# Optimization experiments

Hardware: AMD Instinct MI355X
Metric: run time of the kernel (lower is better)

The kernel has to match this reference:

```python
import jax, jax.numpy as jnp
import numpy as np

B, T, D, H, OUT, VOCAB = 64, 100, 1024, 1024, 28, 28


def setup_inputs() -> dict:
    key = jax.random.key(0)
    ks = jax.random.split(key, 12)
    s = 0.05
    return {
        "x": jax.random.normal(ks[0], (B, T, D), jnp.float32),
        # encoder GRU (keras reset_after=True): kernel [D,3H], recurrent [H,3H], bias [2,3H]
        "enc_W": jax.random.normal(ks[1], (D, 3 * H), jnp.float32) * s,
        "enc_U": jax.random.normal(ks[2], (H, 3 * H), jnp.float32) * s,
        "enc_b": jax.random.normal(ks[3], (2, 3 * H), jnp.float32) * s,
        # AdditiveAttention learned scale vector [H]
        "att_scale": jax.random.normal(ks[4], (H,), jnp.float32) * s,
        # Embedding(28, H)
        "emb_W": jax.random.normal(ks[5], (VOCAB, H), jnp.float32) * s,
        # decoder GRUCell
        "dec_W": jax.random.normal(ks[6], (H, 3 * H), jnp.float32) * s,
        "dec_U": jax.random.normal(ks[7], (H, 3 * H), jnp.float32) * s,
        "dec_b": jax.random.normal(ks[8], (2, 3 * H), jnp.float32) * s,
        # fc: Dense(OUT) on concat([h, context]) -> [2H, OUT]
        "fc_W": jax.random.normal(ks[9], (2 * H, OUT), jnp.float32) * s,
        "fc_b": jax.random.normal(ks[10], (OUT,), jnp.float32) * s,
    }


def _gru_update(x_t, h, W, U, b):
    # keras GRU math with reset_after=True
    mx = x_t @ W + b[0]          # [B,3H]
    mi = h @ U + b[1]            # [B,3H]
    xz, xr, xh = jnp.split(mx, 3, axis=-1)
    rz, rr, rh = jnp.split(mi, 3, axis=-1)
    z = jax.nn.sigmoid(xz + rz)
    r = jax.nn.sigmoid(xr + rr)
    hh = jnp.tanh(xh + r * rh)
    return z * h + (1.0 - z) * hh


def reference(x, enc_W, enc_U, enc_b, att_scale, emb_W, dec_W, dec_U, dec_b, fc_W, fc_b):
    b, t, _ = x.shape
    h = jnp.zeros((b, enc_U.shape[0]), x.dtype)

    # encoder GRU, return_sequences=True
    def enc_step(h, x_t):
        h = _gru_update(x_t, h, enc_W, enc_U, enc_b)
        return h, h

    _, hpe = jax.lax.scan(enc_step, h, jnp.swapaxes(x, 0, 1))  # [T,B,H]
    hpe = jnp.swapaxes(hpe, 0, 1)                              # [B,T,H]

    out_dim = fc_b.shape[0]
    p0 = jnp.zeros((b, out_dim), x.dtype)
    h0 = jnp.zeros((b, dec_U.shape[0]), x.dtype)

    def dec_step(carry, _):
        p, hd = carry
        # additive attention: scores[b,j] = sum_d scale[d]*tanh(q[b,d]+k[b,j,d])
        scores = jnp.einsum('bth,h->bt', jnp.tanh(hd[:, None, :] + hpe), att_scale)
        attn = jax.nn.softmax(scores, axis=-1)
        ctx = jnp.einsum('bt,bth->bh', attn, hpe)
        idx = jnp.argmax(p, axis=-1)          # [B] int
        e = emb_W[idx]                        # [B,H]
        hd = _gru_update(e, hd, dec_W, dec_U, dec_b)
        p = jnp.concatenate([hd, ctx], axis=1) @ fc_W + fc_b
        return (p, hd), p

    _, outs = jax.lax.scan(dec_step, (p0, h0), None, length=t)  # [T,B,OUT]
    return jnp.swapaxes(outs, 0, 1)                              # [B,T,OUT]
```

## Files before the change

### kernel.cpp

```cpp
#include <hip/hip_runtime.h>

#define TT 100
#define HH 1024
#define H3 3072
#define NOUT 28

#define AGENT __HIP_MEMORY_SCOPE_AGENT
#define WGRP  __HIP_MEMORY_SCOPE_WORKGROUP
#define SPIN_CAP (1u<<20)

__device__ __forceinline__ float frcp_(float x){ return __builtin_amdgcn_rcpf(x); }
__device__ __forceinline__ float fsig_(float x){ return frcp_(1.0f + __expf(-x)); }
__device__ __forceinline__ float ftanh_(float x){ return 1.0f - 2.0f*frcp_(__expf(2.0f*x) + 1.0f); }

__device__ __forceinline__ unsigned long long aload8(const unsigned long long* p){
    return __hip_atomic_load(p, __ATOMIC_RELAXED, AGENT);
}
__device__ __forceinline__ unsigned aload4(const int* p){
    return (unsigned)__hip_atomic_load(p, __ATOMIC_RELAXED, AGENT);
}

__device__ __forceinline__ void gridbar(int* slot, int sub, int target){
    __syncthreads();
    if (threadIdx.x == 0){
        __hip_atomic_fetch_add(slot + sub*16, 1, __ATOMIC_RELAXED, AGENT);
        unsigned gy = 0; int s;
        do {
            s = 0;
            #pragma unroll
            for (int c=0;c<16;c++) s += __hip_atomic_load(slot + c*16, __ATOMIC_RELAXED, AGENT);
            if (s < target){ if (++gy > SPIN_CAP) break; __builtin_amdgcn_s_sleep(1); }
        } while (s < target);
    }
    __syncthreads();
}

__device__ __forceinline__ void wbar4(int* c, int tgt){
    asm volatile("s_waitcnt lgkmcnt(0)" ::: "memory");
    if ((threadIdx.x & 63) == 0) __hip_atomic_fetch_add(c, 1, __ATOMIC_RELAXED, WGRP);
    unsigned gy = 0;
    while (__hip_atomic_load(c, __ATOMIC_RELAXED, WGRP) < tgt){ if (++gy > SPIN_CAP) break; }
    asm volatile("" ::: "memory");
}

__global__ void k_init(int* ib, int n){
    int g = blockIdx.x*256 + threadIdx.x;
    if (g < n) ib[g] = 0;
}

__global__ __launch_bounds__(256) void k_transpose(const float* __restrict__ U0,
                                                   const float* __restrict__ U1,
                                                   float* __restrict__ T0,
                                                   float* __restrict__ T1){
    const float* U = blockIdx.z ? U1 : U0;
    float*       T = blockIdx.z ? T1 : T0;
    __shared__ float tile[32][33];
    int tx = threadIdx.x & 31, ty = threadIdx.x >> 5;
    int j0 = blockIdx.x*32, k0 = blockIdx.y*32;
    #pragma unroll
    for (int q=0;q<4;q++){
        int kr = ty + q*8;
        tile[kr][tx] = U[(size_t)(k0+kr)*H3 + j0 + tx];
    }
    __syncthreads();
    #pragma unroll
    for (int q=0;q<4;q++){
        int jr = ty + q*8;
        T[(size_t)(j0+jr)*HH + k0 + tx] = tile[tx][jr];
    }
}

__global__ __launch_bounds__(256) void k_edec(const float* __restrict__ emb,
                                              const float* __restrict__ W,
                                              const float* __restrict__ b0,
                                              float* __restrict__ E){
    int gid = blockIdx.x*256 + threadIdx.x;
    int v = gid / H3, j = gid - v*H3;
    float acc = b0[j];
    const float* er = emb + (size_t)v*HH;
    #pragma unroll 4
    for (int k=0;k<HH;k++) acc = fmaf(er[k], W[(size_t)k*H3 + j], acc);
    E[gid] = acc;
}

__global__ __launch_bounds__(256) void k_mxgemm(const float* __restrict__ A,
                                                const float* __restrict__ W,
                                                const float* __restrict__ b0,
                                                float* __restrict__ MXT){
    __shared__ float aT[32*68];
    __shared__ float bL[32*68];
    int tid = threadIdx.x;
    int row0 = blockIdx.y*64, col0 = blockIdx.x*64;
    int arow = tid>>2, acs = (tid&3)*4;
    int bk   = tid>>3, bcs = (tid&7)*4;
    int ty = tid>>4, tx = tid&15;
    float acc[4][4] = {};
    for (int kk=0; kk<HH; kk+=32){
        #pragma unroll
        for (int i=0;i<2;i++){
            int c = acs + i*16;
            float4 v = *(const float4*)(A + (size_t)(row0+arow)*HH + kk + c);
            aT[(c+0)*68 + arow] = v.x; aT[(c+1)*68 + arow] = v.y;
            aT[(c+2)*68 + arow] = v.z; aT[(c+3)*68 + arow] = v.w;
        }
        #pragma unroll
        for (int i=0;i<2;i++){
            int c = bcs + i*32;
            float4 v = *(const float4*)(W + (size_t)(kk+bk)*H3 + col0 + c);
            *(float4*)(bL + bk*68 + c) = v;
        }
        __syncthreads();
        #pragma unroll
        for (int k=0;k<32;k++){
            float4 a4 = *(const float4*)(aT + k*68 + ty*4);
            float4 b4 = *(const float4*)(bL + k*68 + tx*4);
            acc[0][0]=fmaf(a4.x,b4.x,acc[0][0]); acc[0][1]=fmaf(a4.x,b4.y,acc[0][1]);
            acc[0][2]=fmaf(a4.x,b4.z,acc[0][2]); acc[0][3]=fmaf(a4.x,b4.w,acc[0][3]);
            acc[1][0]=fmaf(a4.y,b4.x,acc[1][0]); acc[1][1]=fmaf(a4.y,b4.y,acc[1][1]);
            acc[1][2]=fmaf(a4.y,b4.z,acc[1][2]); acc[1][3]=fmaf(a4.y,b4.w,acc[1][3]);
            acc[2][0]=fmaf(a4.z,b4.x,acc[2][0]); acc[2][1]=fmaf(a4.z,b4.y,acc[2][1]);
            acc[2][2]=fmaf(a4.z,b4.z,acc[2][2]); acc[2][3]=fmaf(a4.z,b4.w,acc[2][3]);
            acc[3][0]=fmaf(a4.w,b4.x,acc[3][0]); acc[3][1]=fmaf(a4.w,b4.y,acc[3][1]);
            acc[3][2]=fmaf(a4.w,b4.z,acc[3][2]); acc[3][3]=fmaf(a4.w,b4.w,acc[3][3]);
        }
        __syncthreads();
    }
    float4 bb = *(const float4*)(b0 + col0 + tx*4);
    #pragma unroll
    for (int i=0;i<4;i++){
        int r = row0 + ty*4 + i;
        int bq = r / 100; int tq = r - bq*100;
        float v0 = acc[i][0] + bb.x, v1 = acc[i][1] + bb.y;
        float v2 = acc[i][2] + bb.z, v3 = acc[i][3] + bb.w;
        float* dst = MXT + ((size_t)tq*H3 + col0 + tx*4)*64 + bq;
        dst[0]   = v0; dst[64]  = v1; dst[128] = v2; dst[192] = v3;
    }
}

__global__ __launch_bounds__(256) void k_enc(const float* __restrict__ MXT,
                                             const float* __restrict__ Ut,
                                             const float* __restrict__ b1,
                                             float* __restrict__ hpe,
                                             float* __restrict__ hT,
                                             int* __restrict__ bar){
    __shared__ float hs[2][16384];
    int tid = threadIdx.x, lane = tid & 63;
    int wg = blockIdx.x;
    int sub = wg & 15;
    int cu = __builtin_amdgcn_readfirstlane(wg*4 + (tid>>6));
    const float* Uz = Ut + (size_t)cu*HH;
    const float* Ur = Uz + (size_t)HH*HH;
    const float* Uh = Ur + (size_t)HH*HH;
    float bz = b1[cu], br = b1[cu+HH], bh = b1[cu+2*HH];
    for (int t=0; t<TT; ++t){
        int cur = t & 1;
        const float* mx = MXT + (size_t)t*H3*64;
        float xz = mx[(size_t)cu*64 + lane];
        float xr = mx[(size_t)(cu+HH)*64 + lane];
        float xh = mx[(size_t)(cu+2*HH)*64 + lane];
        float az=0.f, ar=0.f, ah=0.f, hp=0.f;
        if (t > 0){
            const unsigned long long* g8 = (const unsigned long long*)(hT + (size_t)cur*65536);
            unsigned long long sv[32];
            #pragma unroll
            for (int s=0;s<32;s++) sv[s] = aload8(g8 + s*256 + tid);
            #pragma unroll
            for (int s=0;s<32;s++) ((unsigned long long*)hs[0])[s*256 + tid] = sv[s];
            __syncthreads();
            for (int q=0;q<4;++q){
                if (q<3){
                    #pragma unroll
                    for (int s=0;s<32;s++) sv[s] = aload8(g8 + (q+1)*8192 + s*256 + tid);
                }
                const float* hb = hs[q&1];
                const float* Uzq = Uz + q*256;
                const float* Urq = Ur + q*256;
                const float* Uhq = Uh + q*256;
                #pragma unroll 8
                for (int k=0;k<256;++k){
                    float h = hb[k*64 + lane];
                    az = fmaf(h, Uzq[k], az);
                    ar = fmaf(h, Urq[k], ar);
                    ah = fmaf(h, Uhq[k], ah);
                }
                if ((cu>>8) == q) hp = hb[(cu&255)*64 + lane];
                if (q<3){
                    #pragma unroll
                    for (int s=0;s<32;s++) ((unsigned long long*)hs[(q+1)&1])[s*256 + tid] = sv[s];
                }
                __syncthreads();
            }
        }
        float z  = fsig_(xz + az + bz);
        float r  = fsig_(xr + ar + br);
        float hh = ftanh_(xh + r*(ah + bh));
        float hnew = z*hp + (1.f - z)*hh;
        __hip_atomic_store(hT + (size_t)(cur^1)*65536 + cu*64 + lane, hnew, __ATOMIC_RELAXED, AGENT);
        hpe[((size_t)lane*TT + t)*HH + cu] = hnew;
        gridbar(bar + (size_t)t*256, sub, 256);
    }
}

__global__ __launch_bounds__(512) void k_dec(const float* __restrict__ hpe,
                                             const float* __restrict__ Ut,
                                             const float* __restrict__ b1,
                                             const float* __restrict__ Edec,
                                             const float* __restrict__ scale,
                                             const float* __restrict__ fcW,
                                             const float* __restrict__ fcb,
                                             float* __restrict__ hdT,
                                             float* __restrict__ hdl,
                                             float* __restrict__ out,
                                             int* __restrict__ idx_t,
                                             int* __restrict__ bar,
                                             int* __restrict__ flagidx){
    __shared__ float hs[2][16384];
    __shared__ float ctxs[4][1024];
    __shared__ float m_s[4], S_s[4];
    __shared__ int c_a, c_fc, go, cstg;
    int tid = threadIdx.x, wg = blockIdx.x;
    if (tid == 0){ c_a=0; c_fc=0; go=0; cstg=0; }
    __syncthreads();

    if (tid < 256){
        int lane = tid & 63;
        int sub = wg & 15;
        int cu = __builtin_amdgcn_readfirstlane(wg*4 + (tid>>6));
        const float* Uz = Ut + (size_t)cu*HH;
        const float* Ur = Uz + (size_t)HH*HH;
        const float* Uh = Ur + (size_t)HH*HH;
        float bz = b1[cu], br = b1[cu+HH], bh = b1[cu+2*HH];
        int stgt = 0;
        for (int i=0; i<TT; ++i){
            int cur = i & 1;
            float az=0.f, ar=0.f, ah=0.f, hp=0.f;
            if (i > 0){
                const unsigned long long* g8 = (const unsigned long long*)(hdT + (size_t)cur*65536);
                unsigned long long sv[32];
                #pragma unroll
                for (int s=0;s<32;s++) sv[s] = aload8(g8 + s*256 + tid);
                #pragma unroll
                for (int s=0;s<32;s++) ((unsigned long long*)hs[0])[s*256 + tid] = sv[s];
                wbar4(&cstg, stgt += 4);
                for (int q=0;q<4;++q){
                    if (q<3){
                        #pragma unroll
                        for (int s=0;s<32;s++) sv[s] = aload8(g8 + (q+1)*8192 + s*256 + tid);
                    }
                    const float* hb = hs[q&1];
                    const float* Uzq = Uz + q*256;
                    const float* Urq = Ur + q*256;
                    const float* Uhq = Uh + q*256;
                    #pragma unroll 8
                    for (int k=0;k<256;++k){
                        float h = hb[k*64 + lane];
                        az = fmaf(h, Uzq[k], az);
                        ar = fmaf(h, Urq[k], ar);
                        ah = fmaf(h, Uhq[k], ah);
                    }
                    if ((cu>>8) == q) hp = hb[(cu&255)*64 + lane];
                    if (q<3){
                        #pragma unroll
                        for (int s=0;s<32;s++) ((unsigned long long*)hs[(q+1)&1])[s*256 + tid] = sv[s];
                    }
                    wbar4(&cstg, stgt += 4);
                }
            }
            if (tid == 0){
                unsigned gy = 0; int s;
                do {
                    s = 0;
                    #pragma unroll
                    for (int c=0;c<8;c++) s += __hip_atomic_load(flagidx + (size_t)i*128 + c*16, __ATOMIC_RELAXED, AGENT);
                    if (s < 64){ if (++gy > SPIN_CAP) break; __builtin_amdgcn_s_sleep(1); }
                } while (s < 64);
                __hip_atomic_store(&go, i+1, __ATOMIC_RELAXED, WGRP);
            }
            { unsigned gy=0; while (__hip_atomic_load(&go, __ATOMIC_RELAXED, WGRP) < i+1){ if (++gy > SPIN_CAP) break; } }
            asm volatile("" ::: "memory");
            unsigned mi = aload4(idx_t + (size_t)i*64 + lane);
            if (mi > 27u) mi = 0;
            const float* ed = Edec + (size_t)mi*H3;
            float xz = ed[cu], xr = ed[cu+HH], xh = ed[cu+2*HH];
            float z  = fsig_(xz + az + bz);
            float r  = fsig_(xr + ar + br);
            float hh = ftanh_(xh + r*(ah + bh));
            float hnew = z*hp + (1.f - z)*hh;
            __hip_atomic_store(hdT + (size_t)(cur^1)*65536 + cu*64 + lane, hnew, __ATOMIC_RELAXED, AGENT);
            __hip_atomic_store(hdl + (size_t)(cur^1)*65536 + (size_t)lane*HH + cu, hnew, __ATOMIC_RELAXED, AGENT);
            gridbar(bar + (size_t)i*256, sub, 256);
        }
    } else if (wg < 64){
        int t2 = tid - 256;
        int w = t2 >> 6, lane = t2 & 63, b = wg;
        float sc[16];
        #pragma unroll
        for (int s4=0;s4<4;s4++){
            float4 v = *(const float4*)(scale + lane*16 + s4*4);
            sc[s4*4+0]=v.x; sc[s4*4+1]=v.y; sc[s4*4+2]=v.z; sc[s4*4+3]=v.w;
        }
        int j0 = w*25;
        for (int i=0; i<TT; ++i){
            float q[16];
            if (i == 0){
                #pragma unroll
                for (int d=0;d<16;d++) q[d]=0.f;
            } else {
                const unsigned long long* hq8 = (const unsigned long long*)(hdl + (size_t)(i&1)*65536 + (size_t)b*HH) + lane*8;
                #pragma unroll
                for (int s8=0;s8<8;s8++){
                    unsigned long long v = aload8(hq8 + s8);
                    q[2*s8+0] = __uint_as_float((unsigned)v);
                    q[2*s8+1] = __uint_as_float((unsigned)(v>>32));
                }
            }
            if (w == 0){
                if (i > 0){
                    float acc[NOUT];
                    #pragma unroll
                    for (int o=0;o<NOUT;o++) acc[o]=0.f;
                    float cv[16];
                    #pragma unroll
                    for (int s4=0;s4<4;s4++){
                        float4 c0 = ((const float4*)ctxs[0])[lane*4+s4];
                        float4 c1 = ((const float4*)ctxs[1])[lane*4+s4];
                        float4 c2 = ((const float4*)ctxs[2])[lane*4+s4];
                        float4 c3 = ((const float4*)ctxs[3])[lane*4+s4];
                        cv[s4*4+0]=c0.x+c1.x+c2.x+c3.x;
                        cv[s4*4+1]=c0.y+c1.y+c2.y+c3.y;
                        cv[s4*4+2]=c0.z+c1.z+c2.z+c3.z;
                        cv[s4*4+3]=c0.w+c1.w+c2.w+c3.w;
                    }
                    #pragma unroll
                    for (int dd=0;dd<16;++dd){
                        int d = lane*16 + dd;
                        const float* w0p = fcW + (size_t)d*NOUT;
                        const float* w1p = fcW + (size_t)(d+HH)*NOUT;
                        float hv=q[dd], cvv=cv[dd];
                        #pragma unroll
                        for (int o=0;o<NOUT;o++) acc[o] = fmaf(hv, w0p[o], fmaf(cvv, w1p[o], acc[o]));
                    }
                    #pragma unroll
                    for (int o=0;o<NOUT;o++){
                        #pragma unroll
                        for (int m=1;m<64;m<<=1) acc[o] += __shfl_xor(acc[o], m);
                    }
                    float bv=-3.0e38f; int bi=0;
                    #pragma unroll
                    for (int o=0;o<NOUT;o++){
                        float p = acc[o] + fcb[o];
                        acc[o] = p;
                        if (p > bv){ bv = p; bi = o; }
                    }
                    float vout = 0.f;
                    #pragma unroll
                    for (int o=0;o<NOUT;o++) if (lane == o) vout = acc[o];
                    if (lane < NOUT) out[((size_t)b*TT + (i-1))*NOUT + lane] = vout;
                    if (lane == 0){
                        __hip_atomic_store(idx_t + (size_t)i*64 + b, bi, __ATOMIC_RELAXED, AGENT);
                        asm volatile("s_waitcnt vmcnt(0)" ::: "memory");
                    }
                }
                if (lane == 0){
                    __hip_atomic_fetch_add(flagidx + (size_t)i*128 + (b&7)*16, 1, __ATOMIC_RELAXED, AGENT);
                    __hip_atomic_fetch_add(&c_fc, 1, __ATOMIC_RELAXED, WGRP);
                }
            }
            float m = -3.0e38f, S = 0.f;
            float a[16];
            #pragma unroll
            for (int d=0;d<16;d++) a[d]=0.f;
            for (int jj=0;jj<25;jj++){
                int j = j0 + jj;
                const float* hpj = hpe + ((size_t)b*TT + j)*HH + lane*16;
                float va[16];
                {
                    float4 v0 = *(const float4*)(hpj);
                    float4 v1 = *(const float4*)(hpj+4);
                    float4 v2 = *(const float4*)(hpj+8);
                    float4 v3 = *(const float4*)(hpj+12);
                    va[0]=v0.x;va[1]=v0.y;va[2]=v0.z;va[3]=v0.w;
                    va[4]=v1.x;va[5]=v1.y;va[6]=v1.z;va[7]=v1.w;
                    va[8]=v2.x;va[9]=v2.y;va[10]=v2.z;va[11]=v2.w;
                    va[12]=v3.x;va[13]=v3.y;va[14]=v3.z;va[15]=v3.w;
                }
                float s = 0.f;
                #pragma unroll
                for (int d=0;d<16;d++) s += sc[d]*ftanh_(q[d] + va[d]);
                #pragma unroll
                for (int mm=1;mm<64;mm<<=1) s += __shfl_xor(s, mm);
                float mn = fmaxf(m, s);
                float fold = __expf(m - mn);
                float e = __expf(s - mn);
                S = S*fold + e;
                #pragma unroll
                for (int d=0;d<16;d++) a[d] = a[d]*fold + e*va[d];
                m = mn;
            }
            if (lane == 0){ m_s[w] = m; S_s[w] = S; }
            asm volatile("s_waitcnt lgkmcnt(0)" ::: "memory");
            if (lane == 0) __hip_atomic_fetch_add(&c_a, 1, __ATOMIC_RELAXED, WGRP);
            { unsigned gy=0; while (__hip_atomic_load(&c_a, __ATOMIC_RELAXED, WGRP) < 4*(i+1)){ if (++gy > SPIN_CAP) break; } }
            asm volatile("" ::: "memory");
            float M = fmaxf(fmaxf(m_s[0],m_s[1]), fmaxf(m_s[2],m_s[3]));
            float St = S_s[0]*__expf(m_s[0]-M) + S_s[1]*__expf(m_s[1]-M)
                     + S_s[2]*__expf(m_s[2]-M) + S_s[3]*__expf(m_s[3]-M);
            float g = __expf(m - M) * frcp_(St);
            { unsigned gy=0; while (__hip_atomic_load(&c_fc, __ATOMIC_RELAXED, WGRP) < i+1){ if (++gy > SPIN_CAP) break; } }
            asm volatile("" ::: "memory");
            #pragma unroll
            for (int s4=0;s4<4;s4++){
                float4 o4;
                o4.x=a[s4*4+0]*g; o4.y=a[s4*4+1]*g;
                o4.z=a[s4*4+2]*g; o4.w=a[s4*4+3]*g;
                ((float4*)ctxs[w])[lane*4 + s4] = o4;
            }
            gridbar(bar + (size_t)i*256, wg & 15, 256);
        }
        if (w == 0){
            const unsigned long long* hq8 = (const unsigned long long*)(hdl + (size_t)b*HH) + lane*8;
            float q[16];
            #pragma unroll
            for (int s8=0;s8<8;s8++){
                unsigned long long v = aload8(hq8 + s8);
                q[2*s8+0] = __uint_as_float((unsigned)v);
                q[2*s8+1] = __uint_as_float((unsigned)(v>>32));
            }
            float acc[NOUT];
            #pragma unroll
            for (int o=0;o<NOUT;o++) acc[o]=0.f;
            float cv[16];
            #pragma unroll
            for (int s4=0;s4<4;s4++){
                float4 c0 = ((const float4*)ctxs[0])[lane*4+s4];
                float4 c1 = ((const float4*)ctxs[1])[lane*4+s4];
                float4 c2 = ((const float4*)ctxs[2])[lane*4+s4];
                float4 c3 = ((const float4*)ctxs[3])[lane*4+s4];
                cv[s4*4+0]=c0.x+c1.x+c2.x+c3.x;
                cv[s4*4+1]=c0.y+c1.y+c2.y+c3.y;
                cv[s4*4+2]=c0.z+c1.z+c2.z+c3.z;
                cv[s4*4+3]=c0.w+c1.w+c2.w+c3.w;
            }
            #pragma unroll
            for (int dd=0;dd<16;++dd){
                int d = lane*16 + dd;
                const float* w0p = fcW + (size_t)d*NOUT;
                const float* w1p = fcW + (size_t)(d+HH)*NOUT;
                float hv=q[dd], cvv=cv[dd];
                #pragma unroll
                for (int o=0;o<NOUT;o++) acc[o] = fmaf(hv, w0p[o], fmaf(cvv, w1p[o], acc[o]));
            }
            #pragma unroll
            for (int o=0;o<NOUT;o++){
                #pragma unroll
                for (int m=1;m<64;m<<=1) acc[o] += __shfl_xor(acc[o], m);
            }
            float vout = 0.f;
            #pragma unroll
            for (int o=0;o<NOUT;o++) if (lane == o) vout = acc[o] + fcb[o];
            if (lane < NOUT) out[((size_t)b*TT + 99)*NOUT + lane] = vout;
        }
    } else {
        for (int i=0;i<TT;++i) gridbar(bar + (size_t)i*256, wg & 15, 256);
    }
}

extern "C" void kernel_launch(void* const* d_in, const int* in_sizes, int n_in,
                              void* d_out, int out_size, void* d_ws, size_t ws_size,
                              hipStream_t stream){
    (void)in_sizes; (void)n_in; (void)out_size; (void)ws_size;
    const float* x     = (const float*)d_in[0];
    const float* encW  = (const float*)d_in[1];
    const float* encU  = (const float*)d_in[2];
    const float* encb  = (const float*)d_in[3];
    const float* scale = (const float*)d_in[4];
    const float* emb   = (const float*)d_in[5];
    const float* decW  = (const float*)d_in[6];
    const float* decU  = (const float*)d_in[7];
    const float* decb  = (const float*)d_in[8];
    const float* fcW   = (const float*)d_in[9];
    const float* fcb   = (const float*)d_in[10];
    float* out = (float*)d_out;
    float* ws  = (float*)d_ws;

    float* MXT   = ws;
    float* hdT   = MXT;
    float* hdl   = MXT + 131072;
    float* encUt = MXT   + 19660800;
    float* decUt = encUt + 3145728;
    float* hpe   = decUt + 3145728;
    float* Edec  = hpe   + 6553600;
    float* hT    = Edec  + 86016;
    int*   ib    = (int*)(hT + 131072);
    int*   bar_enc = ib;
    int*   bar_dec = ib + 25600;
    int*   flagidx = ib + 51200;
    int*   idx_t   = ib + 64000;

    const float* encb1 = encb + H3;
    const float* decb1 = decb + H3;

    k_init<<<276,256,0,stream>>>(ib, 70400);
    k_transpose<<<dim3(96,32,2),256,0,stream>>>(encU, decU, encUt, decUt);
    k_edec<<<336,256,0,stream>>>(emb, decW, decb, Edec);
    k_mxgemm<<<dim3(48,100),256,0,stream>>>(x, encW, encb, MXT);
    k_enc<<<256,256,0,stream>>>(MXT, encUt, encb1, hpe, hT, bar_enc);
    k_dec<<<256,512,0,stream>>>(hpe, decUt, decb1, Edec, scale, fcW, fcb,
                                hdT, hdl, out, idx_t, bar_dec, flagidx);
}
```

Before: 10.90 ms.

## Shrink recurrent grids, compute two hidden units per wave with vectorized weights

New measurement: 18.00 ms. +65.1%, slower.

```diff
diff --git a/kernel.cpp b/kernel.cpp
--- a/kernel.cpp
+++ b/kernel.cpp
@@ -7,11 +7,14 @@
 
 #define AGENT __HIP_MEMORY_SCOPE_AGENT
 #define WGRP  __HIP_MEMORY_SCOPE_WORKGROUP
-#define SPIN_CAP (1u<<20)
+#define GB_CAP  (1u<<13)
+#define LDS_CAP (1u<<20)
+#define FL_CAP  (1u<<16)
 
 __device__ __forceinline__ float frcp_(float x){ return __builtin_amdgcn_rcpf(x); }
 __device__ __forceinline__ float fsig_(float x){ return frcp_(1.0f + __expf(-x)); }
 __device__ __forceinline__ float ftanh_(float x){ return 1.0f - 2.0f*frcp_(__expf(2.0f*x) + 1.0f); }
+__device__ __forceinline__ void wait_vm(){ asm volatile("s_waitcnt vmcnt(0)" ::: "memory"); }
 
 __device__ __forceinline__ unsigned long long aload8(const unsigned long long* p){
     return __hip_atomic_load(p, __ATOMIC_RELAXED, AGENT);
@@ -21,6 +24,7 @@
 }
 
 __device__ __forceinline__ void gridbar(int* slot, int sub, int target){
+    wait_vm();
     __syncthreads();
     if (threadIdx.x == 0){
         __hip_atomic_fetch_add(slot + sub*16, 1, __ATOMIC_RELAXED, AGENT);
@@ -29,18 +33,10 @@
             s = 0;
             #pragma unroll
             for (int c=0;c<16;c++) s += __hip_atomic_load(slot + c*16, __ATOMIC_RELAXED, AGENT);
-            if (s < target){ if (++gy > SPIN_CAP) break; __builtin_amdgcn_s_sleep(1); }
+            if (s < target){ if (++gy > GB_CAP) break; __builtin_amdgcn_s_sleep(1); }
         } while (s < target);
     }
     __syncthreads();
-}
-
-__device__ __forceinline__ void wbar4(int* c, int tgt){
-    asm volatile("s_waitcnt lgkmcnt(0)" ::: "memory");
-    if ((threadIdx.x & 63) == 0) __hip_atomic_fetch_add(c, 1, __ATOMIC_RELAXED, WGRP);
-    unsigned gy = 0;
-    while (__hip_atomic_load(c, __ATOMIC_RELAXED, WGRP) < tgt){ if (++gy > SPIN_CAP) break; }
-    asm volatile("" ::: "memory");
 }
 
 __global__ void k_init(int* ib, int n){
@@ -137,67 +133,92 @@
     }
 }
 
-__global__ __launch_bounds__(256) void k_enc(const float* __restrict__ MXT,
+__global__ __launch_bounds__(512) void k_enc(const float* __restrict__ MXT,
                                              const float* __restrict__ Ut,
                                              const float* __restrict__ b1,
                                              float* __restrict__ hpe,
-                                             float* __restrict__ hT,
+                                             float* __restrict__ g_h,
                                              int* __restrict__ bar){
     __shared__ float hs[2][16384];
-    int tid = threadIdx.x, lane = tid & 63;
-    int wg = blockIdx.x;
-    int sub = wg & 15;
-    int cu = __builtin_amdgcn_readfirstlane(wg*4 + (tid>>6));
-    const float* Uz = Ut + (size_t)cu*HH;
-    const float* Ur = Uz + (size_t)HH*HH;
-    const float* Uh = Ur + (size_t)HH*HH;
-    float bz = b1[cu], br = b1[cu+HH], bh = b1[cu+2*HH];
+    int tid = threadIdx.x, lane = tid & 63, wg = blockIdx.x, sub = wg & 15;
+    int cu0 = __builtin_amdgcn_readfirstlane(wg*16 + (tid>>6)*2);
+    int cu1 = cu0 + 1;
+    const float* Uz0 = Ut + (size_t)cu0*HH;
+    const float* Ur0 = Uz0 + (size_t)HH*HH;
+    const float* Uh0 = Ur0 + (size_t)HH*HH;
+    const float* Uz1 = Ut + (size_t)cu1*HH;
+    const float* Ur1 = Uz1 + (size_t)HH*HH;
+    const float* Uh1 = Ur1 + (size_t)HH*HH;
+    float bz0 = b1[cu0], br0 = b1[cu0+HH], bh0 = b1[cu0+2*HH];
+    float bz1 = b1[cu1], br1 = b1[cu1+HH], bh1 = b1[cu1+2*HH];
     for (int t=0; t<TT; ++t){
-        int cur = t & 1;
         const float* mx = MXT + (size_t)t*H3*64;
-        float xz = mx[(size_t)cu*64 + lane];
-        float xr = mx[(size_t)(cu+HH)*64 + lane];
-        float xh = mx[(size_t)(cu+2*HH)*64 + lane];
-        float az=0.f, ar=0.f, ah=0.f, hp=0.f;
+        float xz0 = mx[(size_t)cu0*64 + lane];
+        float xr0 = mx[(size_t)(cu0+HH)*64 + lane];
+        float xh0 = mx[(size_t)(cu0+2*HH)*64 + lane];
+        float xz1 = mx[(size_t)cu1*64 + lane];
+        float xr1 = mx[(size_t)(cu1+HH)*64 + lane];
+        float xh1 = mx[(size_t)(cu1+2*HH)*64 + lane];
+        float az0=0.f, ar0=0.f, ah0=0.f, az1=0.f, ar1=0.f, ah1=0.f, hp0=0.f, hp1=0.f;
         if (t > 0){
-            const unsigned long long* g8 = (const unsigned long long*)(hT + (size_t)cur*65536);
-            unsigned long long sv[32];
+            const unsigned long long* g8 = (const unsigned long long*)(g_h + (size_t)(t&1)*65536);
+            unsigned long long sv[16];
             #pragma unroll
-            for (int s=0;s<32;s++) sv[s] = aload8(g8 + s*256 + tid);
+            for (int s=0;s<16;s++) sv[s] = aload8(g8 + s*512 + tid);
             #pragma unroll
-            for (int s=0;s<32;s++) ((unsigned long long*)hs[0])[s*256 + tid] = sv[s];
+            for (int s=0;s<16;s++) ((unsigned long long*)hs[0])[s*512 + tid] = sv[s];
             __syncthreads();
             for (int q=0;q<4;++q){
                 if (q<3){
                     #pragma unroll
-                    for (int s=0;s<32;s++) sv[s] = aload8(g8 + (q+1)*8192 + s*256 + tid);
+                    for (int s=0;s<16;s++) sv[s] = aload8(g8 + (q+1)*8192 + s*512 + tid);
                 }
                 const float* hb = hs[q&1];
-                const float* Uzq = Uz + q*256;
-                const float* Urq = Ur + q*256;
-                const float* Uhq = Uh + q*256;
-                #pragma unroll 8
-                for (int k=0;k<256;++k){
-                    float h = hb[k*64 + lane];
-                    az = fmaf(h, Uzq[k], az);
-                    ar = fmaf(h, Urq[k], ar);
-                    ah = fmaf(h, Uhq[k], ah);
-                }
-                if ((cu>>8) == q) hp = hb[(cu&255)*64 + lane];
+                const float* Uz0q = Uz0 + q*256; const float* Ur0q = Ur0 + q*256; const float* Uh0q = Uh0 + q*256;
+                const float* Uz1q = Uz1 + q*256; const float* Ur1q = Ur1 + q*256; const float* Uh1q = Uh1 + q*256;
+                #pragma unroll 4
+                for (int k4=0;k4<64;++k4){
+                    float4 uz0 = *(const float4*)(Uz0q + k4*4);
+                    float4 ur0 = *(const float4*)(Ur0q + k4*4);
+                    float4 uh0 = *(const float4*)(Uh0q + k4*4);
+                    float4 uz1 = *(const float4*)(Uz1q + k4*4);
+                    float4 ur1 = *(const float4*)(Ur1q + k4*4);
+                    float4 uh1 = *(const float4*)(Uh1q + k4*4);
+                    float h0 = hb[(k4*4+0)*64 + lane];
+                    float h1 = hb[(k4*4+1)*64 + lane];
+                    float h2 = hb[(k4*4+2)*64 + lane];
+                    float h3 = hb[(k4*4+3)*64 + lane];
+                    az0=fmaf(h0,uz0.x,az0); ar0=fmaf(h0,ur0.x,ar0); ah0=fmaf(h0,uh0.x,ah0);
+                    az1=fmaf(h0,uz1.x,az1); ar1=fmaf(h0,ur1.x,ar1); ah1=fmaf(h0,uh1.x,ah1);
+                    az0=fmaf(h1,uz0.y,az0); ar0=fmaf(h1,ur0.y,ar0); ah0=fmaf(h1,uh0.y,ah0);
+                    az1=fmaf(h1,uz1.y,az1); ar1=fmaf(h1,ur1.y,ar1); ah1=fmaf(h1,uh1.y,ah1);
+                    az0=fmaf(h2,uz0.z,az0); ar0=fmaf(h2,ur0.z,ar0); ah0=fmaf(h2,uh0.z,ah0);
+                    az1=fmaf(h2,uz1.z,az1); ar1=fmaf(h2,ur1.z,ar1); ah1=fmaf(h2,uh1.z,ah1);
+                    az0=fmaf(h3,uz0.w,az0); ar0=fmaf(h3,ur0.w,ar0); ah0=fmaf(h3,uh0.w,ah0);
+                    az1=fmaf(h3,uz1.w,az1); ar1=fmaf(h3,ur1.w,ar1); ah1=fmaf(h3,uh1.w,ah1);
+                }
+                if ((cu0>>8) == q){ hp0 = hb[(cu0&255)*64 + lane]; hp1 = hb[(cu1&255)*64 + lane]; }
                 if (q<3){
                     #pragma unroll
-                    for (int s=0;s<32;s++) ((unsigned long long*)hs[(q+1)&1])[s*256 + tid] = sv[s];
+                    for (int s=0;s<16;s++) ((unsigned long long*)hs[(q+1)&1])[s*512 + tid] = sv[s];
                 }
                 __syncthreads();
             }
         }
-        float z  = fsig_(xz + az + bz);
-        float r  = fsig_(xr + ar + br);
-        float hh = ftanh_(xh + r*(ah + bh));
-        float hnew = z*hp + (1.f - z)*hh;
-        __hip_atomic_store(hT + (size_t)(cur^1)*65536 + cu*64 + lane, hnew, __ATOMIC_RELAXED, AGENT);
-        hpe[((size_t)lane*TT + t)*HH + cu] = hnew;
-        gridbar(bar + (size_t)t*256, sub, 256);
+        float z0  = fsig_(xz0 + az0 + bz0);
+        float r0  = fsig_(xr0 + ar0 + br0);
+        float hh0 = ftanh_(xh0 + r0*(ah0 + bh0));
+        float h0n = z0*hp0 + (1.f - z0)*hh0;
+        float z1  = fsig_(xz1 + az1 + bz1);
+        float r1  = fsig_(xr1 + ar1 + br1);
+        float hh1 = ftanh_(xh1 + r1*(ah1 + bh1));
+        float h1n = z1*hp1 + (1.f - z1)*hh1;
+        int slot = (t+1)&1;
+        __hip_atomic_store(g_h + (size_t)slot*65536 + cu0*64 + lane, h0n, __ATOMIC_RELAXED, AGENT);
+        __hip_atomic_store(g_h + (size_t)slot*65536 + cu1*64 + lane, h1n, __ATOMIC_RELAXED, AGENT);
+        hpe[((size_t)lane*TT + t)*HH + cu0] = h0n;
+        hpe[((size_t)lane*TT + t)*HH + cu1] = h1n;
+        gridbar(bar + (size_t)t*256, sub, 64);
     }
 }
 
@@ -208,8 +229,8 @@
                                              const float* __restrict__ scale,
                                              const float* __restrict__ fcW,
                                              const float* __restrict__ fcb,
-                                             float* __restrict__ hdT,
-                                             float* __restrict__ hdl,
+                                             float* __restrict__ g_hT,
+                                             float* __restrict__ g_hl,
                                              float* __restrict__ out,
                                              int* __restrict__ idx_t,
                                              int* __restrict__ bar,
@@ -217,53 +238,68 @@
     __shared__ float hs[2][16384];
     __shared__ float ctxs[4][1024];
     __shared__ float m_s[4], S_s[4];
-    __shared__ int c_a, c_fc, go, cstg;
-    int tid = threadIdx.x, wg = blockIdx.x;
-    if (tid == 0){ c_a=0; c_fc=0; go=0; cstg=0; }
+    __shared__ int c_a, c_fc, go;
+    int tid = threadIdx.x, wg = blockIdx.x, sub = wg & 15;
+    if (tid == 0){ c_a=0; c_fc=0; go=0; }
     __syncthreads();
 
-    if (tid < 256){
+    if (wg < 64){
         int lane = tid & 63;
-        int sub = wg & 15;
-        int cu = __builtin_amdgcn_readfirstlane(wg*4 + (tid>>6));
-        const float* Uz = Ut + (size_t)cu*HH;
-        const float* Ur = Uz + (size_t)HH*HH;
-        const float* Uh = Ur + (size_t)HH*HH;
-        float bz = b1[cu], br = b1[cu+HH], bh = b1[cu+2*HH];
-        int stgt = 0;
+        int cu0 = __builtin_amdgcn_readfirstlane(wg*16 + (tid>>6)*2);
+        int cu1 = cu0 + 1;
+        const float* Uz0 = Ut + (size_t)cu0*HH;
+        const float* Ur0 = Uz0 + (size_t)HH*HH;
+        const float* Uh0 = Ur0 + (size_t)HH*HH;
+        const float* Uz1 = Ut + (size_t)cu1*HH;
+        const float* Ur1 = Uz1 + (size_t)HH*HH;
+        const float* Uh1 = Ur1 + (size_t)HH*HH;
+        float bz0 = b1[cu0], br0 = b1[cu0+HH], bh0 = b1[cu0+2*HH];
+        float bz1 = b1[cu1], br1 = b1[cu1+HH], bh1 = b1[cu1+2*HH];
         for (int i=0; i<TT; ++i){
-            int cur = i & 1;
-            float az=0.f, ar=0.f, ah=0.f, hp=0.f;
+            float az0=0.f, ar0=0.f, ah0=0.f, az1=0.f, ar1=0.f, ah1=0.f, hp0=0.f, hp1=0.f;
             if (i > 0){
-                const unsigned long long* g8 = (const unsigned long long*)(hdT + (size_t)cur*65536);
-                unsigned long long sv[32];
-                #pragma unroll
-                for (int s=0;s<32;s++) sv[s] = aload8(g8 + s*256 + tid);
-                #pragma unroll
-                for (int s=0;s<32;s++) ((unsigned long long*)hs[0])[s*256 + tid] = sv[s];
-                wbar4(&cstg, stgt += 4);
+                const unsigned long long* g8 = (const unsigned long long*)(g_hT + (size_t)(i&1)*65536);
+                unsigned long long sv[16];
+                #pragma unroll
+                for (int s=0;s<16;s++) sv[s] = aload8(g8 + s*512 + tid);
+                #pragma unroll
+                for (int s=0;s<16;s++) ((unsigned long long*)hs[0])[s*512 + tid] = sv[s];
+                __syncthreads();
                 for (int q=0;q<4;++q){
                     if (q<3){
                         #pragma unroll
-                        for (int s=0;s<32;s++) sv[s] = aload8(g8 + (q+1)*8192 + s*256 + tid);
+                        for (int s=0;s<16;s++) sv[s] = aload8(g8 + (q+1)*8192 + s*512 + tid);
                     }
                     const float* hb = hs[q&1];
-                    const float* Uzq = Uz + q*256;
-                    const float* Urq = Ur + q*256;
-                    const float* Uhq = Uh + q*256;
-                    #pragma unroll 8
-                    for (int k=0;k<256;++k){
-                        float h = hb[k*64 + lane];
-                        az = fmaf(h, Uzq[k], az);
-                        ar = fmaf(h, Urq[k], ar);
-                        ah = fmaf(h, Uhq[k], ah);
-                    }
-                    if ((cu>>8) == q) hp = hb[(cu&255)*64 + lane];
+                    const float* Uz0q = Uz0 + q*256; const float* Ur0q = Ur0 + q*256; const float* Uh0q = Uh0 + q*256;
+                    const float* Uz1q = Uz1 + q*256; const float* Ur1q = Ur1 + q*256; const float* Uh1q = Uh1 + q*256;
+                    #pragma unroll 4
+                    for (int k4=0;k4<64;++k4){
+                        float4 uz0 = *(const float4*)(Uz0q + k4*4);
+                        float4 ur0 = *(const float4*)(Ur0q + k4*4);
+                        float4 uh0 = *(const float4*)(Uh0q + k4*4);
+                        float4 uz1 = *(const float4*)(Uz1q + k4*4);
+                        float4 ur1 = *(const float4*)(Ur1q + k4*4);
+                        float4 uh1 = *(const float4*)(Uh1q + k4*4);
+                        float h0 = hb[(k4*4+0)*64 + lane];
+                        float h1 = hb[(k4*4+1)*64 + lane];
+                        float h2 = hb[(k4*4+2)*64 + lane];
+                        float h3 = hb[(k4*4+3)*64 + lane];
+                        az0=fmaf(h0,uz0.x,az0); ar0=fmaf(h0,ur0.x,ar0); ah0=fmaf(h0,uh0.x,ah0);
+                        az1=fmaf(h0,uz1.x,az1); ar1=fmaf(h0,ur1.x,ar1); ah1=fmaf(h0,uh1.x,ah1);
+                        az0=fmaf(h1,uz0.y,az0); ar0=fmaf(h1,ur0.y,ar0); ah0=fmaf(h1,uh0.y,ah0);
+                        az1=fmaf(h1,uz1.y,az1); ar1=fmaf(h1,ur1.y,ar1); ah1=fmaf(h1,uh1.y,ah1);
+                        az0=fmaf(h2,uz0.z,az0); ar0=fmaf(h2,ur0.z,ar0); ah0=fmaf(h2,uh0.z,ah0);
+                        az1=fmaf(h2,uz1.z,az1); ar1=fmaf(h2,ur1.z,ar1); ah1=fmaf(h2,uh1.z,ah1);
+                        az0=fmaf(h3,uz0.w,az0); ar0=fmaf(h3,ur0.w,ar0); ah0=fmaf(h3,uh0.w,ah0);
+                        az1=fmaf(h3,uz1.w,az1); ar1=fmaf(h3,ur1.w,ar1); ah1=fmaf(h3,uh1.w,ah1);
+                    }
+                    if ((cu0>>8) == q){ hp0 = hb[(cu0&255)*64 + lane]; hp1 = hb[(cu1&255)*64 + lane]; }
                     if (q<3){
                         #pragma unroll
-                        for (int s=0;s<32;s++) ((unsigned long long*)hs[(q+1)&1])[s*256 + tid] = sv[s];
-                    }
-                    wbar4(&cstg, stgt += 4);
+                        for (int s=0;s<16;s++) ((unsigned long long*)hs[(q+1)&1])[s*512 + tid] = sv[s];
+                    }
+                    __syncthreads();
                 }
             }
             if (tid == 0){
@@ -272,196 +308,206 @@
                     s = 0;
                     #pragma unroll
                     for (int c=0;c<8;c++) s += __hip_atomic_load(flagidx + (size_t)i*128 + c*16, __ATOMIC_RELAXED, AGENT);
-                    if (s < 64){ if (++gy > SPIN_CAP) break; __builtin_amdgcn_s_sleep(1); }
+                    if (s < 64){ if (++gy > FL_CAP) break; __builtin_amdgcn_s_sleep(1); }
                 } while (s < 64);
                 __hip_atomic_store(&go, i+1, __ATOMIC_RELAXED, WGRP);
             }
-            { unsigned gy=0; while (__hip_atomic_load(&go, __ATOMIC_RELAXED, WGRP) < i+1){ if (++gy > SPIN_CAP) break; } }
+            { unsigned gy=0; while (__hip_atomic_load(&go, __ATOMIC_RELAXED, WGRP) < i+1){ if (++gy > LDS_CAP) break; } }
             asm volatile("" ::: "memory");
             unsigned mi = aload4(idx_t + (size_t)i*64 + lane);
             if (mi > 27u) mi = 0;
             const float* ed = Edec + (size_t)mi*H3;
-            float xz = ed[cu], xr = ed[cu+HH], xh = ed[cu+2*HH];
-            float z  = fsig_(xz + az + bz);
-            float r  = fsig_(xr + ar + br);
-            float hh = ftanh_(xh + r*(ah + bh));
-            float hnew = z*hp + (1.f - z)*hh;
-            __hip_atomic_store(hdT + (size_t)(cur^1)*65536 + cu*64 + lane, hnew, __ATOMIC_RELAXED, AGENT);
-            __hip_atomic_store(hdl + (size_t)(cur^1)*65536 + (size_t)lane*HH + cu, hnew, __ATOMIC_RELAXED, AGENT);
-            gridbar(bar + (size_t)i*256, sub, 256);
+            float xz0 = ed[cu0], xr0 = ed[cu0+HH], xh0 = ed[cu0+2*HH];
+            float xz1 = ed[cu1], xr1 = ed[cu1+HH], xh1 = ed[cu1+2*HH];
+            float z0  = fsig_(xz0 + az0 + bz0);
+            float r0  = fsig_(xr0 + ar0 + br0);
+            float hh0 = ftanh_(xh0 + r0*(ah0 + bh0));
+            float h0n = z0*hp0 + (1.f - z0)*hh0;
+            float z1  = fsig_(xz1 + az1 + bz1);
+            float r1  = fsig_(xr1 + ar1 + br1);
+            float hh1 = ftanh_(xh1 + r1*(ah1 + bh1));
+            float h1n = z1*hp1 + (1.f - z1)*hh1;
+            int slot = (i&1)^1;
+            __hip_atomic_store(g_hT + (size_t)slot*65536 + cu0*64 + lane, h0n, __ATOMIC_RELAXED, AGENT);
+            __hip_atomic_store(g_hT + (size_t)slot*65536 + cu1*64 + lane, h1n, __ATOMIC_RELAXED, AGENT);
+            __hip_atomic_store(g_hl + (size_t)slot*65536 + (size_t)lane*HH + cu0, h0n, __ATOMIC_RELAXED, AGENT);
+            __hip_atomic_store(g_hl + (size_t)slot*65536 + (size_t)lane*HH + cu1, h1n, __ATOMIC_RELAXED, AGENT);
+            gridbar(bar + (size_t)i*256, sub, 128);
         }
-    } else if (wg < 64){
-        int t2 = tid - 256;
-        int w = t2 >> 6, lane = t2 & 63, b = wg;
-        float sc[16];
-        #pragma unroll
-        for (int s4=0;s4<4;s4++){
-            float4 v = *(const float4*)(scale + lane*16 + s4*4);
-            sc[s4*4+0]=v.x; sc[s4*4+1]=v.y; sc[s4*4+2]=v.z; sc[s4*4+3]=v.w;
-        }
-        int j0 = w*25;
-        for (int i=0; i<TT; ++i){
-            float q[16];
-            if (i == 0){
-                #pragma unroll
-                for (int d=0;d<16;d++) q[d]=0.f;
-            } else {
-                const unsigned long long* hq8 = (const unsigned long long*)(hdl + (size_t)(i&1)*65536 + (size_t)b*HH) + lane*8;
+    } else {
+        int b = wg - 64;
+        if (tid < 256){
+            int w = tid >> 6, lane = tid & 63;
+            float sc[16];
+            #pragma unroll
+            for (int s4=0;s4<4;s4++){
+                float4 v = *(const float4*)(scale + lane*16 + s4*4);
+                sc[s4*4+0]=v.x; sc[s4*4+1]=v.y; sc[s4*4+2]=v.z; sc[s4*4+3]=v.w;
+            }
+            int j0 = w*25;
+            for (int i=0; i<TT; ++i){
+                float q[16];
+                if (i == 0){
+                    #pragma unroll
+                    for (int d=0;d<16;d++) q[d]=0.f;
+                } else {
+                    const unsigned long long* hq8 = (const unsigned long long*)(g_hl + (size_t)(i&1)*65536 + (size_t)b*HH) + lane*8;
+                    #pragma unroll
+                    for (int s8=0;s8<8;s8++){
+                        unsigned long long v = aload8(hq8 + s8);
+                        q[2*s8+0] = __uint_as_float((unsigned)v);
+                        q[2*s8+1] = __uint_as_float((unsigned)(v>>32));
+                    }
+                }
+                if (w == 0){
+                    if (i > 0){
+                        float acc[NOUT];
+                        #pragma unroll
+                        for (int o=0;o<NOUT;o++) acc[o]=0.f;
+                        float cv[16];
+                        #pragma unroll
+                        for (int s4=0;s4<4;s4++){
+                            float4 c0 = ((const float4*)ctxs[0])[lane*4+s4];
+                            float4 c1 = ((const float4*)ctxs[1])[lane*4+s4];
+                            float4 c2 = ((const float4*)ctxs[2])[lane*4+s4];
+                            float4 c3 = ((const float4*)ctxs[3])[lane*4+s4];
+                            cv[s4*4+0]=c0.x+c1.x+c2.x+c3.x;
+                            cv[s4*4+1]=c0.y+c1.y+c2.y+c3.y;
+                            cv[s4*4+2]=c0.z+c1.z+c2.z+c3.z;
+                            cv[s4*4+3]=c0.w+c1.w+c2.w+c3.w;
+                        }
+                        #pragma unroll
+                        for (int dd=0;dd<16;++dd){
+                            int d = lane*16 + dd;
+                            const float* w0p = fcW + (size_t)d*NOUT;
+                            const float* w1p = fcW + (size_t)(d+HH)*NOUT;
+                            float hv=q[dd], cvv=cv[dd];
+                            #pragma unroll
+                            for (int o=0;o<NOUT;o++) acc[o] = fmaf(hv, w0p[o], fmaf(cvv, w1p[o], acc[o]));
+                        }
+                        #pragma unroll
+                        for (int o=0;o<NOUT;o++){
+                            #pragma unroll
+                            for (int m=1;m<64;m<<=1) acc[o] += __shfl_xor(acc[o], m);
+                        }
+                        float bv=-3.0e38f; int bi=0;
+                        #pragma unroll
+                        for (int o=0;o<NOUT;o++){
+                            float p = acc[o] + fcb[o];
+                            acc[o] = p;
+                            if (p > bv){ bv = p; bi = o; }
+                        }
+                        float vout = 0.f;
+                        #pragma unroll
+                        for (int o=0;o<NOUT;o++) if (lane == o) vout = acc[o];
+                        if (lane < NOUT) out[((size_t)b*TT + (i-1))*NOUT + lane] = vout;
+                        if (lane == 0){
+                            __hip_atomic_store(idx_t + (size_t)i*64 + b, bi, __ATOMIC_RELAXED, AGENT);
+                            wait_vm();
+                        }
+                    }
+                    if (lane == 0){
+                        __hip_atomic_fetch_add(flagidx + (size_t)i*128 + (b&7)*16, 1, __ATOMIC_RELAXED, AGENT);
+                        __hip_atomic_fetch_add(&c_fc, 1, __ATOMIC_RELAXED, WGRP);
+                    }
+                }
+                float m = -3.0e38f, S = 0.f;
+                float a[16];
+                #pragma unroll
+                for (int d=0;d<16;d++) a[d]=0.f;
+                for (int jj=0;jj<25;jj++){
+                    int j = j0 + jj;
+                    const float* hpj = hpe + ((size_t)b*TT + j)*HH + lane*16;
+                    float va[16];
+                    {
+                        float4 v0 = *(const float4*)(hpj);
+                        float4 v1 = *(const float4*)(hpj+4);
+                        float4 v2 = *(const float4*)(hpj+8);
+                        float4 v3 = *(const float4*)(hpj+12);
+                        va[0]=v0.x;va[1]=v0.y;va[2]=v0.z;va[3]=v0.w;
+                        va[4]=v1.x;va[5]=v1.y;va[6]=v1.z;va[7]=v1.w;
+                        va[8]=v2.x;va[9]=v2.y;va[10]=v2.z;va[11]=v2.w;
+                        va[12]=v3.x;va[13]=v3.y;va[14]=v3.z;va[15]=v3.w;
+                    }
+                    float s = 0.f;
+                    #pragma unroll
+                    for (int d=0;d<16;d++) s += sc[d]*ftanh_(q[d] + va[d]);
+                    #pragma unroll
+                    for (int mm=1;mm<64;mm<<=1) s += __shfl_xor(s, mm);
+                    float mn = fmaxf(m, s);
+                    float fold = __expf(m - mn);
+                    float e = __expf(s - mn);
+                    S = S*fold + e;
+                    #pragma unroll
+                    for (int d=0;d<16;d++) a[d] = a[d]*fold + e*va[d];
+                    m = mn;
+                }
+                if (lane == 0){ m_s[w] = m; S_s[w] = S; }
+                asm volatile("s_waitcnt lgkmcnt(0)" ::: "memory");
+                if (lane == 0) __hip_atomic_fetch_add(&c_a, 1, __ATOMIC_RELAXED, WGRP);
+                { unsigned gy=0; while (__hip_atomic_load(&c_a, __ATOMIC_RELAXED, WGRP) < 4*(i+1)){ if (++gy > LDS_CAP) break; } }
+                asm volatile("" ::: "memory");
+                float M = fmaxf(fmaxf(m_s[0],m_s[1]), fmaxf(m_s[2],m_s[3]));
+                float St = S_s[0]*__expf(m_s[0]-M) + S_s[1]*__expf(m_s[1]-M)
+                         + S_s[2]*__expf(m_s[2]-M) + S_s[3]*__expf(m_s[3]-M);
+                float g = __expf(m - M) * frcp_(St);
+                { unsigned gy=0; while (__hip_atomic_load(&c_fc, __ATOMIC_RELAXED, WGRP) < i+1){ if (++gy > LDS_CAP) break; } }
+                asm volatile("" ::: "memory");
+                #pragma unroll
+                for (int s4=0;s4<4;s4++){
+                    float4 o4;
+                    o4.x=a[s4*4+0]*g; o4.y=a[s4*4+1]*g;
+                    o4.z=a[s4*4+2]*g; o4.w=a[s4*4+3]*g;
+                    ((float4*)ctxs[w])[lane*4 + s4] = o4;
+                }
+                gridbar(bar + (size_t)i*256, sub, 128);
+            }
+            if (w == 0){
+                const unsigned long long* hq8 = (const unsigned long long*)(g_hl + (size_t)b*HH) + lane*8;
+                float q[16];
                 #pragma unroll
                 for (int s8=0;s8<8;s8++){
                     unsigned long long v = aload8(hq8 + s8);
                     q[2*s8+0] = __uint_as_float((unsigned)v);
                     q[2*s8+1] = __uint_as_float((unsigned)(v>>32));
                 }
+                float acc[NOUT];
+                #pragma unroll
+                for (int o=0;o<NOUT;o++) acc[o]=0.f;
+                float cv[16];
+                #pragma unroll
+                for (int s4=0;s4<4;s4++){
+                    float4 c0 = ((const float4*)ctxs[0])[lane*4+s4];
+                    float4 c1 = ((const float4*)ctxs[1])[lane*4+s4];
+                    float4 c2 = ((const float4*)ctxs[2])[lane*4+s4];
+                    float4 c3 = ((const float4*)ctxs[3])[lane*4+s4];
+                    cv[s4*4+0]=c0.x+c1.x+c2.x+c3.x;
+                    cv[s4*4+1]=c0.y+c1.y+c2.y+c3.y;
+                    cv[s4*4+2]=c0.z+c1.z+c2.z+c3.z;
+                    cv[s4*4+3]=c0.w+c1.w+c2.w+c3.w;
+                }
+                #pragma unroll
+                for (int dd=0;dd<16;++dd){
+                    int d = lane*16 + dd;
+                    const float* w0p = fcW + (size_t)d*NOUT;
+                    const float* w1p = fcW + (size_t)(d+HH)*NOUT;
+                    float hv=q[dd], cvv=cv[dd];
+                    #pragma unroll
+                    for (int o=0;o<NOUT;o++) acc[o] = fmaf(hv, w0p[o], fmaf(cvv, w1p[o], acc[o]));
+                }
+                #pragma unroll
+                for (int o=0;o<NOUT;o++){
+                    #pragma unroll
+                    for (int m=1;m<64;m<<=1) acc[o] += __shfl_xor(acc[o], m);
+                }
+                float vout = 0.f;
+                #pragma unroll
+                for (int o=0;o<NOUT;o++) if (lane == o) vout = acc[o] + fcb[o];
+                if (lane < NOUT) out[((size_t)b*TT + 99)*NOUT + lane] = vout;
             }
-            if (w == 0){
-                if (i > 0){
-                    float acc[NOUT];
-                    #pragma unroll
-                    for (int o=0;o<NOUT;o++) acc[o]=0.f;
-                    float cv[16];
-                    #pragma unroll
-                    for (int s4=0;s4<4;s4++){
-                        float4 c0 = ((const float4*)ctxs[0])[lane*4+s4];
-                        float4 c1 = ((const float4*)ctxs[1])[lane*4+s4];
-                        float4 c2 = ((const float4*)ctxs[2])[lane*4+s4];
-                        float4 c3 = ((const float4*)ctxs[3])[lane*4+s4];
-                        cv[s4*4+0]=c0.x+c1.x+c2.x+c3.x;
-                        cv[s4*4+1]=c0.y+c1.y+c2.y+c3.y;
-                        cv[s4*4+2]=c0.z+c1.z+c2.z+c3.z;
-                        cv[s4*4+3]=c0.w+c1.w+c2.w+c3.w;
-                    }
-                    #pragma unroll
-                    for (int dd=0;dd<16;++dd){
-                        int d = lane*16 + dd;
-                        const float* w0p = fcW + (size_t)d*NOUT;
-                        const float* w1p = fcW + (size_t)(d+HH)*NOUT;
-                        float hv=q[dd], cvv=cv[dd];
-                        #pragma unroll
-                        for (int o=0;o<NOUT;o++) acc[o] = fmaf(hv, w0p[o], fmaf(cvv, w1p[o], acc[o]));
-                    }
-                    #pragma unroll
-                    for (int o=0;o<NOUT;o++){
-                        #pragma unroll
-                        for (int m=1;m<64;m<<=1) acc[o] += __shfl_xor(acc[o], m);
-                    }
-                    float bv=-3.0e38f; int bi=0;
-                    #pragma unroll
-                    for (int o=0;o<NOUT;o++){
-                        float p = acc[o] + fcb[o];
-                        acc[o] = p;
-                        if (p > bv){ bv = p; bi = o; }
-                    }
-                    float vout = 0.f;
-                    #pragma unroll
-                    for (int o=0;o<NOUT;o++) if (lane == o) vout = acc[o];
-                    if (lane < NOUT) out[((size_t)b*TT + (i-1))*NOUT + lane] = vout;
-                    if (lane == 0){
-                        __hip_atomic_store(idx_t + (size_t)i*64 + b, bi, __ATOMIC_RELAXED, AGENT);
-                        asm volatile("s_waitcnt vmcnt(0)" ::: "memory");
-                    }
-                }
-                if (lane == 0){
-                    __hip_atomic_fetch_add(flagidx + (size_t)i*128 + (b&7)*16, 1, __ATOMIC_RELAXED, AGENT);
-                    __hip_atomic_fetch_add(&c_fc, 1, __ATOMIC_RELAXED, WGRP);
-                }
-            }
-            float m = -3.0e38f, S = 0.f;
-            float a[16];
-            #pragma unroll
-            for (int d=0;d<16;d++) a[d]=0.f;
-            for (int jj=0;jj<25;jj++){
-                int j = j0 + jj;
-                const float* hpj = hpe + ((size_t)b*TT + j)*HH + lane*16;
-                float va[16];
-                {
-                    float4 v0 = *(const float4*)(hpj);
-                    float4 v1 = *(const float4*)(hpj+4);
-                    float4 v2 = *(const float4*)(hpj+8);
-                    float4 v3 = *(const float4*)(hpj+12);
-                    va[0]=v0.x;va[1]=v0.y;va[2]=v0.z;va[3]=v0.w;
-                    va[4]=v1.x;va[5]=v1.y;va[6]=v1.z;va[7]=v1.w;
-                    va[8]=v2.x;va[9]=v2.y;va[10]=v2.z;va[11]=v2.w;
-                    va[12]=v3.x;va[13]=v3.y;va[14]=v3.z;va[15]=v3.w;
-                }
-                float s = 0.f;
-                #pragma unroll
-                for (int d=0;d<16;d++) s += sc[d]*ftanh_(q[d] + va[d]);
-                #pragma unroll
-                for (int mm=1;mm<64;mm<<=1) s += __shfl_xor(s, mm);
-                float mn = fmaxf(m, s);
-                float fold = __expf(m - mn);
-                float e = __expf(s - mn);
-                S = S*fold + e;
-                #pragma unroll
-                for (int d=0;d<16;d++) a[d] = a[d]*fold + e*va[d];
-                m = mn;
-            }
-            if (lane == 0){ m_s[w] = m; S_s[w] = S; }
-            asm volatile("s_waitcnt lgkmcnt(0)" ::: "memory");
-            if (lane == 0) __hip_atomic_fetch_add(&c_a, 1, __ATOMIC_RELAXED, WGRP);
-            { unsigned gy=0; while (__hip_atomic_load(&c_a, __ATOMIC_RELAXED, WGRP) < 4*(i+1)){ if (++gy > SPIN_CAP) break; } }
-            asm volatile("" ::: "memory");
-            float M = fmaxf(fmaxf(m_s[0],m_s[1]), fmaxf(m_s[2],m_s[3]));
-            float St = S_s[0]*__expf(m_s[0]-M) + S_s[1]*__expf(m_s[1]-M)
-                     + S_s[2]*__expf(m_s[2]-M) + S_s[3]*__expf(m_s[3]-M);
-            float g = __expf(m - M) * frcp_(St);
-            { unsigned gy=0; while (__hip_atomic_load(&c_fc, __ATOMIC_RELAXED, WGRP) < i+1){ if (++gy > SPIN_CAP) break; } }
-            asm volatile("" ::: "memory");
-            #pragma unroll
-            for (int s4=0;s4<4;s4++){
-                float4 o4;
-                o4.x=a[s4*4+0]*g; o4.y=a[s4*4+1]*g;
-                o4.z=a[s4*4+2]*g; o4.w=a[s4*4+3]*g;
-                ((float4*)ctxs[w])[lane*4 + s4] = o4;
-            }
-            gridbar(bar + (size_t)i*256, wg & 15, 256);
+        } else {
+            for (int i=0;i<TT;++i) gridbar(bar + (size_t)i*256, sub, 128);
         }
-        if (w == 0){
-            const unsigned long long* hq8 = (const unsigned long long*)(hdl + (size_t)b*HH) + lane*8;
-            float q[16];
-            #pragma unroll
-            for (int s8=0;s8<8;s8++){
-                unsigned long long v = aload8(hq8 + s8);
-                q[2*s8+0] = __uint_as_float((unsigned)v);
-                q[2*s8+1] = __uint_as_float((unsigned)(v>>32));
-            }
-            float acc[NOUT];
-            #pragma unroll
-            for (int o=0;o<NOUT;o++) acc[o]=0.f;
-            float cv[16];
-            #pragma unroll
-            for (int s4=0;s4<4;s4++){
-                float4 c0 = ((const float4*)ctxs[0])[lane*4+s4];
-                float4 c1 = ((const float4*)ctxs[1])[lane*4+s4];
-                float4 c2 = ((const float4*)ctxs[2])[lane*4+s4];
-                float4 c3 = ((const float4*)ctxs[3])[lane*4+s4];
-                cv[s4*4+0]=c0.x+c1.x+c2.x+c3.x;
-                cv[s4*4+1]=c0.y+c1.y+c2.y+c3.y;
-                cv[s4*4+2]=c0.z+c1.z+c2.z+c3.z;
-                cv[s4*4+3]=c0.w+c1.w+c2.w+c3.w;
-            }
-            #pragma unroll
-            for (int dd=0;dd<16;++dd){
-                int d = lane*16 + dd;
-                const float* w0p = fcW + (size_t)d*NOUT;
-                const float* w1p = fcW + (size_t)(d+HH)*NOUT;
-                float hv=q[dd], cvv=cv[dd];
-                #pragma unroll
-                for (int o=0;o<NOUT;o++) acc[o] = fmaf(hv, w0p[o], fmaf(cvv, w1p[o], acc[o]));
-            }
-            #pragma unroll
-            for (int o=0;o<NOUT;o++){
-                #pragma unroll
-                for (int m=1;m<64;m<<=1) acc[o] += __shfl_xor(acc[o], m);
-            }
-            float vout = 0.f;
-            #pragma unroll
-            for (int o=0;o<NOUT;o++) if (lane == o) vout = acc[o] + fcb[o];
-            if (lane < NOUT) out[((size_t)b*TT + 99)*NOUT + lane] = vout;
-        }
-    } else {
-        for (int i=0;i<TT;++i) gridbar(bar + (size_t)i*256, wg & 15, 256);
     }
 }
 
@@ -484,14 +530,14 @@
     float* ws  = (float*)d_ws;
 
     float* MXT   = ws;
-    float* hdT   = MXT;
-    float* hdl   = MXT + 131072;
+    float* g_hdT = MXT;
+    float* g_hdl = MXT + 131072;
     float* encUt = MXT   + 19660800;
     float* decUt = encUt + 3145728;
     float* hpe   = decUt + 3145728;
     float* Edec  = hpe   + 6553600;
-    float* hT    = Edec  + 86016;
-    int*   ib    = (int*)(hT + 131072);
+    float* g_hT  = Edec  + 86016;
+    int*   ib    = (int*)(g_hT + 131072);
     int*   bar_enc = ib;
     int*   bar_dec = ib + 25600;
     int*   flagidx = ib + 51200;
@@ -504,7 +550,7 @@
     k_transpose<<<dim3(96,32,2),256,0,stream>>>(encU, decU, encUt, decUt);
     k_edec<<<336,256,0,stream>>>(emb, decW, decb, Edec);
     k_mxgemm<<<dim3(48,100),256,0,stream>>>(x, encW, encb, MXT);
-    k_enc<<<256,256,0,stream>>>(MXT, encUt, encb1, hpe, hT, bar_enc);
-    k_dec<<<256,512,0,stream>>>(hpe, decUt, decb1, Edec, scale, fcW, fcb,
-                                hdT, hdl, out, idx_t, bar_dec, flagidx);
-}
+    k_enc<<<64,512,0,stream>>>(MXT, encUt, encb1, hpe, g_hT, bar_enc);
+    k_dec<<<128,512,0,stream>>>(hpe, decUt, decb1, Edec, scale, fcW, fcb,
+                                g_hdT, g_hdl, out, idx_t, bar_dec, flagidx);
+}
```
